# Kernel optimization log

Hardware: AMD Instinct MI355X
Metric: run time of the kernel (lower is better)

The kernel has to match this reference:

```python
import jax, jax.numpy as jnp
import numpy as np

B, S, D, Fd, M, H, L = 4, 1024, 1024, 4096, 512, 16, 2
HD = D // H
EPS = 1e-5


def _ln(x, s, b):
    m = jnp.mean(x, axis=-1, keepdims=True)
    v = jnp.mean((x - m) ** 2, axis=-1, keepdims=True)
    return (x - m) * jax.lax.rsqrt(v + EPS) * s + b


def _mha(x, Wq, bq, Wk, bk, Wv, bv, Wo, bo):
    b_, s_, _ = x.shape
    Q = (x @ Wq + bq).reshape(b_, s_, H, HD)
    K = (x @ Wk + bk).reshape(b_, s_, H, HD)
    V = (x @ Wv + bv).reshape(b_, s_, H, HD)
    scores = jnp.einsum('bihd,bjhd->bhij', Q, K) / np.sqrt(HD).astype(np.float32)
    w = jax.nn.softmax(scores, axis=-1)
    out = jnp.einsum('bhij,bjhd->bihd', w, V).reshape(b_, s_, D)
    return out @ Wo + bo


def setup_inputs() -> dict:
    key = jax.random.key(0)
    ks = iter(jax.random.split(key, 40))
    w = lambda shape: jax.random.normal(next(ks), shape, jnp.float32) * 0.02
    inp = {
        'x': jax.random.normal(next(ks), (B, S, D), jnp.float32),
        # stacked per-global-layer params [L, ...]
        'Wq': w((L, D, D)), 'bq': jnp.zeros((L, D)),
        'Wk': w((L, D, D)), 'bk': jnp.zeros((L, D)),
        'Wv': w((L, D, D)), 'bv': jnp.zeros((L, D)),
        'Wo': w((L, D, D)), 'bo': jnp.zeros((L, D)),
        'W1': w((L, D, Fd)), 'b1': jnp.zeros((L, Fd)),
        'W2': w((L, Fd, D)), 'b2': jnp.zeros((L, D)),
        'n1s': jnp.ones((L, D)), 'n1b': jnp.zeros((L, D)),
        'n2s': jnp.ones((L, D)), 'n2b': jnp.zeros((L, D)),
        # top-level params
        'ln1s': jnp.ones((D,)), 'ln1b': jnp.zeros((D,)),
        'ln2s': jnp.ones((D,)), 'ln2b': jnp.zeros((D,)),
        'ln3s': jnp.ones((D,)), 'ln3b': jnp.zeros((D,)),
        'Wb': w((D, M)), 'bb': jnp.zeros((M,)),      # backbone stand-in
        'Wm': w((M, D)), 'bm': jnp.zeros((D,)),      # self.linear
        'Wf1': w((D, Fd)), 'bf1': jnp.zeros((Fd,)),  # top feed_forward
        'Wf2': w((Fd, D)), 'bf2': jnp.zeros((D,)),
    }
    return inp


def reference(x, Wq, bq, Wk, bk, Wv, bv, Wo, bo, W1, b1, W2, b2,
              n1s, n1b, n2s, n2b, ln1s, ln1b, ln2s, ln2b, ln3s, ln3b,
              Wb, bb, Wm, bm, Wf1, bf1, Wf2, bf2):
    # dropout is identity (eval mode)
    # global branch: stacked EncoderLayers
    g = x
    for i in range(L):
        a = _mha(g, Wq[i], bq[i], Wk[i], bk[i], Wv[i], bv[i], Wo[i], bo[i])
        g = _ln(g + a, n1s[i], n1b[i])
        ff = jax.nn.relu(g @ W1[i] + b1[i]) @ W2[i] + b2[i]
        g = _ln(g + ff, n2s[i], n2b[i])

    def local(frac):
        st = S // frac
        xs = x[:, -st:, :]
        mo = (xs @ Wb + bb) @ Wm + bm
        y = _ln(xs + mo, ln1s, ln1b)
        return jnp.pad(y, ((0, 0), (S - st, 0), (0, 0)))

    output = g + local(2) + local(4)  # S >= 4 branch
    h = _ln(output + x, ln2s, ln2b)
    ff = jax.nn.relu(output @ Wf1 + bf1) @ Wf2 + bf2
    return _ln(h + ff, ln3s, ln3b)
```

## Files before the change

kernel.cpp:

```cpp
#include <hip/hip_runtime.h>
#include <stdint.h>


typedef short   s16x8 __attribute__((ext_vector_type(8)));
typedef float   f32x4 __attribute__((ext_vector_type(4)));
typedef uint16_t u16x8 __attribute__((ext_vector_type(8)));
typedef uint16_t u16x4 __attribute__((ext_vector_type(4)));

__device__ __forceinline__ float bf2f(uint16_t h) {
    union { uint32_t u; float f; } c; c.u = ((uint32_t)h) << 16; return c.f;
}
__device__ __forceinline__ uint16_t f2bf(float f) {
    union { float f; uint32_t u; } c; c.f = f;
    uint32_t u = c.u;
    u += 0x7fffu + ((u >> 16) & 1u);
    return (uint16_t)(u >> 16);
}

__device__ __forceinline__ void g2l16(const uint16_t* g, uint16_t* l) {
    __builtin_amdgcn_global_load_lds(
        (const __attribute__((address_space(1))) void*)g,
        (__attribute__((address_space(3))) void*)l, 16, 0, 0);
}

template<int MODE, int BN, int BK, int DB>
__global__ __launch_bounds__(256) void gemm_bt(
    const uint16_t* __restrict__ A, const uint16_t* __restrict__ Bt,
    const float* __restrict__ bias0, const float* __restrict__ bias1,
    const float* __restrict__ bias2,
    uint16_t* __restrict__ C0, uint16_t* __restrict__ C1,
    uint16_t* __restrict__ C2,
    int M, int N, int K)
{
    constexpr int JN   = BN / 32;
    constexpr int KS   = BK / 32;
    constexpr int CPR  = BK / 8;
    constexpr int LG   = (BK == 32) ? 2 : 3;
    constexpr int RA   = (128 * BK / 8) / 256;
    constexpr int RB   = (BN  * BK / 8) / 256;
    constexpr int NBUF = DB ? 2 : 1;
    constexpr int STG  = NBUF * (128 + BN) * BK;
    constexpr int EPI  = (MODE == 3) ? 0 : 128 * (BN + 8);
    constexpr int SMEM = (STG > EPI) ? STG : EPI;
    __shared__ __align__(16) uint16_t smem[SMEM];
    uint16_t* sAp = smem;
    uint16_t* sBp = smem + NBUF * 128 * BK;

    const int t    = threadIdx.x;
    const int w    = t >> 6;
    const int lane = t & 63;
    const int qd   = lane >> 4;
    const int cc   = lane & 15;

    int bm, bn;
    {
        int gx = gridDim.x, gy = gridDim.y;
        if ((gy & 7) == 0) {
            int id   = blockIdx.y * gx + blockIdx.x;
            int gpg  = gy >> 3;
            int rest = id >> 3;
            bm = (id & 7) * gpg + rest % gpg;
            bn = rest / gpg;
        } else { bm = blockIdx.y; bn = blockIdx.x; }
    }
    const int m0 = bm * 128;
    const int n0 = bn * BN;
    const int wm = (w >> 1) * 64;
    const int wn = (w & 1) * (BN / 2);

    auto key = [](int row) -> int {
        return (BK == 32) ? ((row >> 1) & 3) : (row & 7);
    };

    f32x4 acc[4][JN];
#pragma unroll
    for (int i = 0; i < 4; ++i)
#pragma unroll
        for (int j = 0; j < JN; ++j) acc[i][j] = (f32x4)0.0f;

    int rA[RA], kA[RA];
#pragma unroll
    for (int is = 0; is < RA; ++is) {
        int gc = is * 256 + t;
        int row = gc >> LG, ph = gc & (CPR - 1);
        rA[is] = row;
        kA[is] = (ph ^ key(row)) * 8;
    }
    int rB[RB], kB[RB];
#pragma unroll
    for (int is = 0; is < RB; ++is) {
        int gc = is * 256 + t;
        int row = gc >> LG, ph = gc & (CPR - 1);
        rB[is] = row;
        kB[is] = (ph ^ key(row)) * 8;
    }
    int offA[4][KS], offB[JN][KS];
#pragma unroll
    for (int i = 0; i < 4; ++i) {
        int ml = wm + i * 16 + cc;
#pragma unroll
        for (int ks = 0; ks < KS; ++ks)
            offA[i][ks] = ml * BK + ((ks * 4 + qd) ^ key(ml)) * 8;
    }
#pragma unroll
    for (int j = 0; j < JN; ++j) {
        int nl = wn + j * 16 + cc;
#pragma unroll
        for (int ks = 0; ks < KS; ++ks)
            offB[j][ks] = nl * BK + ((ks * 4 + qd) ^ key(nl)) * 8;
    }

    auto stage = [&](int kt, int buf) {
#pragma unroll
        for (int is = 0; is < RA; ++is)
            g2l16(A + (size_t)(m0 + rA[is]) * K + kt + kA[is],
                  sAp + (size_t)buf * 128 * BK + (size_t)(is * 256 + w * 64) * 8);
#pragma unroll
        for (int is = 0; is < RB; ++is)
            g2l16(Bt + (size_t)(n0 + rB[is]) * K + kt + kB[is],
                  sBp + (size_t)buf * BN * BK + (size_t)(is * 256 + w * 64) * 8);
    };
    auto compute = [&](int buf) {
        const uint16_t* sa = sAp + (size_t)buf * 128 * BK;
        const uint16_t* sb = sBp + (size_t)buf * BN * BK;
#pragma unroll
        for (int ks = 0; ks < KS; ++ks) {
            s16x8 af[4], bv[JN];
#pragma unroll
            for (int i = 0; i < 4; ++i) af[i] = *(const s16x8*)(sa + offA[i][ks]);
#pragma unroll
            for (int j = 0; j < JN; ++j) bv[j] = *(const s16x8*)(sb + offB[j][ks]);
#pragma unroll
            for (int i = 0; i < 4; ++i)
#pragma unroll
                for (int j = 0; j < JN; ++j)
                    acc[i][j] = __builtin_amdgcn_mfma_f32_16x16x32_bf16(
                        af[i], bv[j], acc[i][j], 0, 0, 0);
        }
    };

    if (DB) {
        stage(0, 0);
        __syncthreads();
        int cur = 0;
        for (int kt = 0; kt < K; kt += BK) {
            if (kt + BK < K) stage(kt + BK, cur ^ 1);
            compute(cur);
            __syncthreads();
            cur ^= 1;
        }
    } else {
        for (int kt = 0; kt < K; kt += BK) {
            stage(kt, 0);
            __syncthreads();
            compute(0);
            __syncthreads();
        }
    }

    if (MODE == 3) {
#pragma unroll
        for (int j = 0; j < JN; ++j) {
            int col = n0 + wn + j * 16 + cc;
            int seg = col >> 10;
            const float* bp = (seg == 0) ? bias0 : (seg == 1) ? bias1 : bias2;
            float bb = bp[col & 1023];
#pragma unroll
            for (int i = 0; i < 4; ++i) {
                f32x4 v = acc[i][j];
#pragma unroll
                for (int r = 0; r < 4; ++r) {
                    float val = v[r] + bb;
                    int row = m0 + wm + i * 16 + qd * 4 + r;
                    if (col < 1024) {
                        C0[(size_t)row * 1024 + col] = f2bf(val);
                    } else if (col < 2048) {
                        C1[(size_t)row * 1024 + (col - 1024)] = f2bf(val);
                    } else {
                        int c = col - 2048;
                        int b = row >> 10, s = row & 1023;
                        int hh = c >> 6, d = c & 63;
                        C2[((size_t)(b * 16 + hh) * 64 + d) * 1024 + s] = f2bf(val);
                    }
                }
            }
        }
    } else {
        constexpr int ST = BN + 8;
#pragma unroll
        for (int j = 0; j < JN; ++j) {
            int col = wn + j * 16 + cc;
            float bb = bias0[n0 + col];
#pragma unroll
            for (int i = 0; i < 4; ++i) {
                f32x4 v = acc[i][j];
#pragma unroll
                for (int r = 0; r < 4; ++r) {
                    float val = v[r] + bb;
                    if (MODE == 1) val = fmaxf(val, 0.0f);
                    smem[(wm + i * 16 + qd * 4 + r) * ST + col] = f2bf(val);
                }
            }
        }
        __syncthreads();
        constexpr int NP  = 128 * BN / 2048;
        constexpr int TPR = BN / 8;
#pragma unroll
        for (int p = 0; p < NP; ++p) {
            int row  = p * (256 / TPR) + t / TPR;
            int colc = (t % TPR) * 8;
            u16x8 v = *(const u16x8*)(smem + row * ST + colc);
            *(u16x8*)(C0 + (size_t)(m0 + row) * N + n0 + colc) = v;
        }
    }
}

#define FA_P 76
__global__ __launch_bounds__(256) void flash_attn(
    const uint16_t* __restrict__ Q, const uint16_t* __restrict__ K,
    const uint16_t* __restrict__ Vt, uint16_t* __restrict__ O)
{
    __shared__ __align__(16) uint16_t Qs[64 * FA_P];
    __shared__ __align__(16) uint16_t Ks[64 * FA_P];
    __shared__ __align__(16) uint16_t Vs[64 * FA_P];
    __shared__ __align__(16) uint16_t Ps[64 * FA_P];

    const int t    = threadIdx.x;
    const int w    = t >> 6;
    const int lane = t & 63;
    const int qd   = lane >> 4;
    const int cc   = lane & 15;
    const int id   = blockIdx.x;
    const int xg   = id & 7;
    const int loc  = id >> 3;
    const int bh   = xg * 8 + (loc >> 4);
    const int qblk = loc & 15;
    const int b    = bh >> 4, hh = bh & 15;
    const size_t rowbase = (size_t)b * 1024;

#pragma unroll
    for (int is = 0; is < 2; ++is) {
        int c = is * 256 + t, r = c >> 3, ch = c & 7;
        *(u16x8*)(Qs + r * FA_P + ch * 8) =
            *(const u16x8*)(Q + (rowbase + qblk * 64 + r) * 1024 + hh * 64 + ch * 8);
    }

    f32x4 o[4];
    float lrow[4] = {0.0f, 0.0f, 0.0f, 0.0f};
#pragma unroll
    for (int j = 0; j < 4; ++j) o[j] = (f32x4)0.0f;

    for (int kb = 0; kb < 1024; kb += 64) {
        __syncthreads();
#pragma unroll
        for (int is = 0; is < 2; ++is) {
            int c = is * 256 + t, r = c >> 3, ch = c & 7;
            *(u16x8*)(Ks + r * FA_P + ch * 8) =
                *(const u16x8*)(K + (rowbase + kb + r) * 1024 + hh * 64 + ch * 8);
            *(u16x8*)(Vs + r * FA_P + ch * 8) =
                *(const u16x8*)(Vt + ((size_t)(bh * 64 + r)) * 1024 + kb + ch * 8);
        }
        __syncthreads();

        f32x4 sc[4];
        s16x8 aq0 = *(const s16x8*)(Qs + (w * 16 + cc) * FA_P + qd * 8);
        s16x8 aq1 = *(const s16x8*)(Qs + (w * 16 + cc) * FA_P + 32 + qd * 8);
#pragma unroll
        for (int j = 0; j < 4; ++j) {
            s16x8 b0 = *(const s16x8*)(Ks + (j * 16 + cc) * FA_P + qd * 8);
            s16x8 b1 = *(const s16x8*)(Ks + (j * 16 + cc) * FA_P + 32 + qd * 8);
            sc[j] = __builtin_amdgcn_mfma_f32_16x16x32_bf16(aq0, b0, (f32x4)0.0f, 0, 0, 0);
            sc[j] = __builtin_amdgcn_mfma_f32_16x16x32_bf16(aq1, b1, sc[j], 0, 0, 0);
        }

#pragma unroll
        for (int r = 0; r < 4; ++r) {
            float p0 = __expf(sc[0][r] * 0.125f);
            float p1 = __expf(sc[1][r] * 0.125f);
            float p2 = __expf(sc[2][r] * 0.125f);
            float p3 = __expf(sc[3][r] * 0.125f);
            lrow[r] += (p0 + p1) + (p2 + p3);
            int prow = (w * 16 + qd * 4 + r) * FA_P + cc;
            Ps[prow]      = f2bf(p0);
            Ps[prow + 16] = f2bf(p1);
            Ps[prow + 32] = f2bf(p2);
            Ps[prow + 48] = f2bf(p3);
        }

#pragma unroll
        for (int ks = 0; ks < 2; ++ks) {
            s16x8 ap = *(const s16x8*)(Ps + (w * 16 + cc) * FA_P + ks * 32 + qd * 8);
#pragma unroll
            for (int j = 0; j < 4; ++j) {
                s16x8 bb = *(const s16x8*)(Vs + (j * 16 + cc) * FA_P + ks * 32 + qd * 8);
                o[j] = __builtin_amdgcn_mfma_f32_16x16x32_bf16(ap, bb, o[j], 0, 0, 0);
            }
        }
    }

#pragma unroll
    for (int r = 0; r < 4; ++r) {
        float rs = lrow[r];
        rs += __shfl_xor(rs, 1);
        rs += __shfl_xor(rs, 2);
        rs += __shfl_xor(rs, 4);
        rs += __shfl_xor(rs, 8);
        float inv = 1.0f / rs;
        size_t grow = rowbase + qblk * 64 + w * 16 + qd * 4 + r;
#pragma unroll
        for (int j = 0; j < 4; ++j)
            O[grow * 1024 + hh * 64 + j * 16 + cc] = f2bf(o[j][r] * inv);
    }
}

template<int BT, int F32OUT>
__global__ __launch_bounds__(256) void ln_res(
    const uint16_t* __restrict__ A, const void* __restrict__ Bp,
    const float* __restrict__ S, const float* __restrict__ Bi,
    void* __restrict__ outp)
{
    const int row = blockIdx.x, t = threadIdx.x;
    const int w = t >> 6, lane = t & 63;
    u16x4 a4 = *(const u16x4*)(A + (size_t)row * 1024 + t * 4);
    float bvals[4];
    if (BT == 0) {
        u16x4 b4 = *(const u16x4*)((const uint16_t*)Bp + (size_t)row * 1024 + t * 4);
#pragma unroll
        for (int e = 0; e < 4; ++e) bvals[e] = bf2f(b4[e]);
    } else {
        float4 b4 = *(const float4*)((const float*)Bp + (size_t)row * 1024 + t * 4);
        bvals[0] = b4.x; bvals[1] = b4.y; bvals[2] = b4.z; bvals[3] = b4.w;
    }
    float v[4], sum = 0.0f, sq = 0.0f;
#pragma unroll
    for (int e = 0; e < 4; ++e) {
        v[e] = bf2f(a4[e]) + bvals[e];
        sum += v[e];
        sq  += v[e] * v[e];
    }
#pragma unroll
    for (int d = 1; d < 64; d <<= 1) {
        sum += __shfl_xor(sum, d);
        sq  += __shfl_xor(sq, d);
    }
    __shared__ float rs[4], rq[4];
    if (lane == 0) { rs[w] = sum; rq[w] = sq; }
    __syncthreads();
    sum = rs[0] + rs[1] + rs[2] + rs[3];
    sq  = rq[0] + rq[1] + rq[2] + rq[3];
    float mean = sum * (1.0f / 1024.0f);
    float var  = sq * (1.0f / 1024.0f) - mean * mean;
    float rstd = rsqrtf(var + 1e-5f);
    float4 s4  = *(const float4*)(S + t * 4);
    float4 bi4 = *(const float4*)(Bi + t * 4);
    float r0 = (v[0] - mean) * rstd * s4.x + bi4.x;
    float r1 = (v[1] - mean) * rstd * s4.y + bi4.y;
    float r2 = (v[2] - mean) * rstd * s4.z + bi4.z;
    float r3 = (v[3] - mean) * rstd * s4.w + bi4.w;
    if (F32OUT) {
        *(float4*)((float*)outp + (size_t)row * 1024 + t * 4) =
            make_float4(r0, r1, r2, r3);
    } else {
        u16x4 o4;
        o4[0] = f2bf(r0); o4[1] = f2bf(r1); o4[2] = f2bf(r2); o4[3] = f2bf(r3);
        *(u16x4*)((uint16_t*)outp + (size_t)row * 1024 + t * 4) = o4;
    }
}

__global__ __launch_bounds__(256) void add3(
    const uint16_t* __restrict__ g, const uint16_t* __restrict__ y2,
    const uint16_t* __restrict__ y4, uint16_t* __restrict__ out)
{
    size_t e = ((size_t)blockIdx.x * 256 + threadIdx.x) * 4;
    int row = (int)(e >> 10), col = (int)(e & 1023);
    int b = row >> 10, s = row & 1023;
    u16x4 gv = *(const u16x4*)(g + e);
    float v[4];
#pragma unroll
    for (int k = 0; k < 4; ++k) v[k] = bf2f(gv[k]);
    if (s >= 512) {
        u16x4 a = *(const u16x4*)(y2 + ((size_t)(b * 512 + s - 512)) * 1024 + col);
#pragma unroll
        for (int k = 0; k < 4; ++k) v[k] += bf2f(a[k]);
    }
    if (s >= 768) {
        u16x4 a = *(const u16x4*)(y4 + ((size_t)(b * 256 + s - 768)) * 1024 + col);
#pragma unroll
        for (int k = 0; k < 4; ++k) v[k] += bf2f(a[k]);
    }
    u16x4 o4;
#pragma unroll
    for (int k = 0; k < 4; ++k) o4[k] = f2bf(v[k]);
    *(u16x4*)(out + e) = o4;
}

__global__ __launch_bounds__(256) void copy_rows_f32(
    const float* __restrict__ x, uint16_t* __restrict__ out, int lgst)
{
    size_t e = ((size_t)blockIdx.x * 256 + threadIdx.x) * 4;
    int row = (int)(e >> 10), col = (int)(e & 1023);
    int st = 1 << lgst;
    int b = row >> lgst, s = row & (st - 1);
    float4 a = *(const float4*)(x + ((size_t)(b * 1024 + (1024 - st) + s)) * 1024 + col);
    u16x4 o4;
    o4[0] = f2bf(a.x); o4[1] = f2bf(a.y); o4[2] = f2bf(a.z); o4[3] = f2bf(a.w);
    *(u16x4*)(out + e) = o4;
}

__global__ __launch_bounds__(256) void transpose_k(
    const float* __restrict__ W, uint16_t* __restrict__ Wt, int Kd, int Nd)
{
    __shared__ uint16_t tile[64][68];
    const int t  = threadIdx.x;
    const int n0 = blockIdx.x * 64, k0 = blockIdx.y * 64;
#pragma unroll
    for (int p = 0; p < 4; ++p) {
        int k  = p * 16 + (t >> 4);
        int nn = (t & 15) * 4;
        float4 a = *(const float4*)(W + (size_t)(k0 + k) * Nd + n0 + nn);
        tile[nn + 0][k] = f2bf(a.x);
        tile[nn + 1][k] = f2bf(a.y);
        tile[nn + 2][k] = f2bf(a.z);
        tile[nn + 3][k] = f2bf(a.w);
    }
    __syncthreads();
#pragma unroll
    for (int p = 0; p < 2; ++p) {
        int nn = p * 32 + (t >> 3);
        int kk = (t & 7) * 8;
        u16x8 o = *(const u16x8*)(&tile[nn][kk]);
        *(u16x8*)(Wt + (size_t)(n0 + nn) * Kd + k0 + kk) = o;
    }
}

__global__ __launch_bounds__(256) void cvt(
    const float* __restrict__ src, uint16_t* __restrict__ dst)
{
    size_t i = ((size_t)blockIdx.x * 256 + threadIdx.x) * 8;
    float4 a = *(const float4*)(src + i);
    float4 b = *(const float4*)(src + i + 4);
    u16x8 o;
    o[0] = f2bf(a.x); o[1] = f2bf(a.y); o[2] = f2bf(a.z); o[3] = f2bf(a.w);
    o[4] = f2bf(b.x); o[5] = f2bf(b.y); o[6] = f2bf(b.z); o[7] = f2bf(b.w);
    *(u16x8*)(dst + i) = o;
}

extern "C" void kernel_launch(void* const* d_in, const int* in_sizes, int n_in,
                              void* d_out, int out_size, void* d_ws, size_t ws_size,
                              hipStream_t stream)
{
    const float* x    = (const float*)d_in[0];
    const float* Wq   = (const float*)d_in[1];
    const float* bq   = (const float*)d_in[2];
    const float* Wk   = (const float*)d_in[3];
    const float* bk   = (const float*)d_in[4];
    const float* Wv   = (const float*)d_in[5];
    const float* bv   = (const float*)d_in[6];
    const float* Wo   = (const float*)d_in[7];
    const float* bo   = (const float*)d_in[8];
    const float* W1   = (const float*)d_in[9];
    const float* b1   = (const float*)d_in[10];
    const float* W2   = (const float*)d_in[11];
    const float* b2   = (const float*)d_in[12];
    const float* n1s  = (const float*)d_in[13];
    const float* n1b  = (const float*)d_in[14];
    const float* n2s  = (const float*)d_in[15];
    const float* n2b  = (const float*)d_in[16];
    const float* ln1s = (const float*)d_in[17];
    const float* ln1b = (const float*)d_in[18];
    const float* ln2s = (const float*)d_in[19];
    const float* ln2b = (const float*)d_in[20];
    const float* ln3s = (const float*)d_in[21];
    const float* ln3b = (const float*)d_in[22];
    const float* Wb   = (const float*)d_in[23];
    const float* bb   = (const float*)d_in[24];
    const float* Wm   = (const float*)d_in[25];
    const float* bm   = (const float*)d_in[26];
    const float* Wf1  = (const float*)d_in[27];
    const float* bf1  = (const float*)d_in[28];
    const float* Wf2  = (const float*)d_in[29];
    const float* bf2  = (const float*)d_in[30];

    char* ws = (char*)d_ws;
    const size_t MB = (size_t)1 << 20;
    uint16_t* g    = (uint16_t*)(ws);
    uint16_t* tb   = (uint16_t*)(ws + 8 * MB);
    char*     big  = ws + 16 * MB;
    uint16_t* qb   = (uint16_t*)(big);
    uint16_t* kbuf = (uint16_t*)(big + 8 * MB);
    uint16_t* vtb  = (uint16_t*)(big + 16 * MB);
    uint16_t* ob   = (uint16_t*)(big + 24 * MB);
    uint16_t* ffb  = (uint16_t*)(big);
    uint16_t* xbf  = (uint16_t*)(ws + 48 * MB);
    uint16_t* hb   = (uint16_t*)(ws + 48 * MB);
    uint16_t* wT   = (uint16_t*)(ws + 56 * MB);

    auto T = [&](const float* Wsrc, int Kd, int Nd, uint16_t* dst) {
        transpose_k<<<dim3(Nd / 64, Kd / 64), 256, 0, stream>>>(Wsrc, dst, Kd, Nd);
    };

    cvt<<<2048, 256, 0, stream>>>(x, xbf);

    const uint16_t* gin = xbf;
    for (int i = 0; i < 2; ++i) {
        const size_t wOff = (size_t)i * 1024 * 1024;
        const size_t fOff = (size_t)i * 1024 * 4096;
        T(Wq + wOff, 1024, 1024, wT);
        T(Wk + wOff, 1024, 1024, wT + (size_t)1024 * 1024);
        T(Wv + wOff, 1024, 1024, wT + (size_t)2048 * 1024);
        gemm_bt<3, 128, 32, 1><<<dim3(24, 32), 256, 0, stream>>>(
            gin, wT, bq + i * 1024, bk + i * 1024, bv + i * 1024,
            qb, kbuf, vtb, 4096, 3072, 1024);
        flash_attn<<<1024, 256, 0, stream>>>(qb, kbuf, vtb, ob);
        T(Wo + wOff, 1024, 1024, wT);
        gemm_bt<0, 64, 64, 1><<<dim3(16, 32), 256, 0, stream>>>(
            ob, wT, bo + i * 1024, nullptr, nullptr, tb, nullptr, nullptr,
            4096, 1024, 1024);
        ln_res<0, 0><<<4096, 256, 0, stream>>>(gin, tb, n1s + i * 1024, n1b + i * 1024, g);
        T(W1 + fOff, 1024, 4096, wT);
        gemm_bt<1, 128, 32, 1><<<dim3(32, 32), 256, 0, stream>>>(
            g, wT, b1 + i * 4096, nullptr, nullptr, ffb, nullptr, nullptr,
            4096, 4096, 1024);
        T(W2 + fOff, 4096, 1024, wT);
        gemm_bt<0, 64, 64, 1><<<dim3(16, 32), 256, 0, stream>>>(
            ffb, wT, b2 + i * 1024, nullptr, nullptr, tb, nullptr, nullptr,
            4096, 1024, 4096);
        ln_res<0, 0><<<4096, 256, 0, stream>>>(g, tb, n2s + i * 1024, n2b + i * 1024, g);
        gin = g;
    }

    uint16_t* xsc = (uint16_t*)(big);
    uint16_t* lk  = (uint16_t*)(big + 8 * MB);
    uint16_t* mo  = (uint16_t*)(big + 16 * MB);
    uint16_t* yy  = (uint16_t*)(big + 24 * MB);
    copy_rows_f32<<<2048, 256, 0, stream>>>(x, xsc, 9);
    copy_rows_f32<<<1024, 256, 0, stream>>>(x, xsc + (size_t)2048 * 1024, 8);
    uint16_t* WbT = wT;
    uint16_t* WmT = wT + (size_t)512 * 1024;
    T(Wb, 1024, 512, WbT);
    T(Wm, 512, 1024, WmT);
    gemm_bt<0, 64, 64, 1><<<dim3(8, 24), 256, 0, stream>>>(
        xsc, WbT, bb, nullptr, nullptr, lk, nullptr, nullptr, 3072, 512, 1024);
    gemm_bt<0, 64, 64, 1><<<dim3(16, 24), 256, 0, stream>>>(
        lk, WmT, bm, nullptr, nullptr, mo, nullptr, nullptr, 3072, 1024, 512);
    ln_res<0, 0><<<3072, 256, 0, stream>>>(xsc, mo, ln1s, ln1b, yy);
    uint16_t* y2 = yy;
    uint16_t* y4 = yy + (size_t)2048 * 1024;

    add3<<<4096, 256, 0, stream>>>(g, y2, y4, g);
    ln_res<1, 0><<<4096, 256, 0, stream>>>(g, x, ln2s, ln2b, hb);
    T(Wf1, 1024, 4096, wT);
    gemm_bt<1, 128, 32, 1><<<dim3(32, 32), 256, 0, stream>>>(
        g, wT, bf1, nullptr, nullptr, ffb, nullptr, nullptr, 4096, 4096, 1024);
    T(Wf2, 4096, 1024, wT);
    gemm_bt<0, 64, 64, 1><<<dim3(16, 32), 256, 0, stream>>>(
        ffb, wT, bf2, nullptr, nullptr, tb, nullptr, nullptr, 4096, 1024, 4096);
    ln_res<0, 1><<<4096, 256, 0, stream>>>(hb, tb, ln3s, ln3b, d_out);
}
```

Measured before the change: 802.7 us.

## Add 256x256-tile 512-thread GEMM with 4-stage pipeline for QKV and FFN1

Adds a new GEMM kernel with 256x256 output tiles, 8 waves, a 4-deep global-to-LDS ring buffer with XOR-swizzled layout, staggered A/B staging interleaved with MFMA phases, and an LDS-staged coalesced epilogue. It replaces the 128-wide tile GEMM for the fused QKV projection and the two K=1024 FFN up-projections. The goal is more data reuse per tile and better overlap of loads with MFMA work. The trade-off is fewer workgroups (192/256) on a 256-CU part, which may leave CUs idle, plus heavy register and LDS use.

```diff
diff --git a/kernel.cpp b/kernel.cpp
--- a/kernel.cpp
+++ b/kernel.cpp
@@ -21,6 +21,195 @@
     __builtin_amdgcn_global_load_lds(
         (const __attribute__((address_space(1))) void*)g,
         (__attribute__((address_space(3))) void*)l, 16, 0, 0);
+}
+
+template<int MODE>
+__global__ __launch_bounds__(512, 2) void gemm256(
+    const uint16_t* __restrict__ A, const uint16_t* __restrict__ Bt,
+    const float* __restrict__ bias0, const float* __restrict__ bias1,
+    const float* __restrict__ bias2,
+    uint16_t* __restrict__ C0, uint16_t* __restrict__ C1,
+    uint16_t* __restrict__ C2,
+    int N)
+{
+    __shared__ __align__(16) uint16_t smem[65536];
+    uint16_t* sA = smem;
+    uint16_t* sB = smem + 32768;
+
+    const int tid  = threadIdx.x;
+    const int lane = tid & 63;
+    const int w    = tid >> 6;
+    const int qd   = lane >> 4;
+    const int cc   = lane & 15;
+    const int wmg  = w >> 2;
+    const int wni  = w & 3;
+    const int wn   = wni * 64;
+    const int wb   = tid & ~63;
+
+    const int nwg = gridDim.x;
+    const int cpx = nwg >> 3;
+    const int id  = blockIdx.x;
+    const int wg  = (id & 7) * cpx + (id >> 3);
+    const int bm  = wg & 15;
+    const int bn  = wg >> 4;
+    const int m0  = bm * 256;
+    const int n0  = bn * 256;
+
+    const float* bp = bias0;
+    int n0c = n0;
+    if (MODE == 3) {
+        int seg = n0 >> 10;
+        n0c = n0 & 1023;
+        bp = (seg == 0) ? bias0 : (seg == 1) ? bias1 : bias2;
+    }
+    float bb[4];
+#pragma unroll
+    for (int j = 0; j < 4; ++j) bb[j] = bp[n0c + wn + j * 16 + cc];
+
+    int offA[8], offB[4];
+#pragma unroll
+    for (int i = 0; i < 8; ++i) {
+        int ml = wmg * 128 + i * 16 + cc;
+        offA[i] = ml * 32 + ((qd ^ ((ml >> 1) & 3)) * 8);
+    }
+#pragma unroll
+    for (int j = 0; j < 4; ++j) {
+        int nl = wn + j * 16 + cc;
+        offB[j] = nl * 32 + ((qd ^ ((nl >> 1) & 3)) * 8);
+    }
+
+    int rS[2], kS[2];
+#pragma unroll
+    for (int is = 0; is < 2; ++is) {
+        int gc = is * 512 + tid;
+        int row = gc >> 2, ph = gc & 3;
+        rS[is] = row;
+        kS[is] = (ph ^ ((row >> 1) & 3)) * 8;
+    }
+    auto stA = [&](int tt) {
+        uint16_t* d = sA + (tt & 3) * 8192;
+        int kt = tt * 32;
+#pragma unroll
+        for (int is = 0; is < 2; ++is)
+            g2l16(A + (size_t)(m0 + rS[is]) * 1024 + kt + kS[is],
+                  d + (size_t)(is * 512 + wb) * 8);
+    };
+    auto stB = [&](int tt) {
+        uint16_t* d = sB + (tt & 3) * 8192;
+        int kt = tt * 32;
+#pragma unroll
+        for (int is = 0; is < 2; ++is)
+            g2l16(Bt + (size_t)(n0 + rS[is]) * 1024 + kt + kS[is],
+                  d + (size_t)(is * 512 + wb) * 8);
+    };
+
+    f32x4 acc[8][4];
+#pragma unroll
+    for (int i = 0; i < 8; ++i)
+#pragma unroll
+        for (int j = 0; j < 4; ++j) acc[i][j] = (f32x4)0.0f;
+
+    stA(0); stB(0); stA(1); stB(1); stA(2); stB(2);
+    asm volatile("s_waitcnt vmcnt(8)" ::: "memory");
+    __builtin_amdgcn_s_barrier();
+
+    s16x8 bv[4];
+#pragma unroll 1
+    for (int t = 0; t < 32; ++t) {
+        const uint16_t* sa = sA + (t & 3) * 8192;
+        const uint16_t* sb = sB + (t & 3) * 8192;
+        if (t < 29) stA(t + 3);
+        s16x8 av[4];
+#pragma unroll
+        for (int j = 0; j < 4; ++j) bv[j] = *(const s16x8*)(sb + offB[j]);
+#pragma unroll
+        for (int i = 0; i < 4; ++i) av[i] = *(const s16x8*)(sa + offA[i]);
+        __builtin_amdgcn_s_barrier();
+        asm volatile("s_waitcnt lgkmcnt(0)" ::: "memory");
+        __builtin_amdgcn_sched_barrier(0);
+        __builtin_amdgcn_s_setprio(1);
+#pragma unroll
+        for (int i = 0; i < 4; ++i)
+#pragma unroll
+            for (int j = 0; j < 4; ++j)
+                acc[i][j] = __builtin_amdgcn_mfma_f32_16x16x32_bf16(
+                    av[i], bv[j], acc[i][j], 0, 0, 0);
+        __builtin_amdgcn_s_setprio(0);
+        __builtin_amdgcn_s_barrier();
+        if (t < 29) stB(t + 3);
+#pragma unroll
+        for (int i = 0; i < 4; ++i) av[i] = *(const s16x8*)(sa + offA[4 + i]);
+        __builtin_amdgcn_s_barrier();
+        asm volatile("s_waitcnt lgkmcnt(0)" ::: "memory");
+        __builtin_amdgcn_sched_barrier(0);
+        __builtin_amdgcn_s_setprio(1);
+#pragma unroll
+        for (int i = 0; i < 4; ++i)
+#pragma unroll
+            for (int j = 0; j < 4; ++j)
+                acc[4 + i][j] = __builtin_amdgcn_mfma_f32_16x16x32_bf16(
+                    av[i], bv[j], acc[4 + i][j], 0, 0, 0);
+        __builtin_amdgcn_s_setprio(0);
+        if (t < 29)       { asm volatile("s_waitcnt vmcnt(8)" ::: "memory"); }
+        else if (t == 29) { asm volatile("s_waitcnt vmcnt(4)" ::: "memory"); }
+        else if (t == 30) { asm volatile("s_waitcnt vmcnt(0)" ::: "memory"); }
+        __builtin_amdgcn_s_barrier();
+    }
+
+    if (MODE == 3 && (n0 >> 10) == 2) {
+#pragma unroll
+        for (int j = 0; j < 4; ++j) {
+            int c = n0c + wn + j * 16 + cc;
+            int hh = c >> 6, d = c & 63;
+#pragma unroll
+            for (int i = 0; i < 8; ++i) {
+                int rb = m0 + wmg * 128 + i * 16 + qd * 4;
+                int b = rb >> 10, s = rb & 1023;
+                u16x4 o;
+#pragma unroll
+                for (int r = 0; r < 4; ++r) o[r] = f2bf(acc[i][j][r] + bb[j]);
+                *(u16x4*)(C2 + ((size_t)((b * 16 + hh) * 64 + d)) * 1024 + s) = o;
+            }
+        }
+        return;
+    }
+    {
+        uint16_t* C = C0;
+        int Nc = N;
+        if (MODE == 3) {
+            int seg = n0 >> 10;
+            C = (seg == 0) ? C0 : C1;
+            Nc = 1024;
+        }
+        constexpr int ST = 264;
+#pragma unroll
+        for (int h = 0; h < 2; ++h) {
+            if (wmg == h) {
+#pragma unroll
+                for (int i = 0; i < 8; ++i)
+#pragma unroll
+                    for (int j = 0; j < 4; ++j) {
+                        f32x4 v = acc[i][j];
+#pragma unroll
+                        for (int r = 0; r < 4; ++r) {
+                            float val = v[r] + bb[j];
+                            if (MODE == 1) val = fmaxf(val, 0.0f);
+                            smem[(i * 16 + qd * 4 + r) * ST + wn + j * 16 + cc] =
+                                f2bf(val);
+                        }
+                    }
+            }
+            __syncthreads();
+#pragma unroll
+            for (int p = 0; p < 8; ++p) {
+                int row  = p * 16 + (tid >> 5);
+                int colc = (tid & 31) * 8;
+                u16x8 v = *(const u16x8*)(smem + row * ST + colc);
+                *(u16x8*)(C + (size_t)(m0 + h * 128 + row) * Nc + n0c + colc) = v;
+            }
+            __syncthreads();
+        }
+    }
 }
 
 template<int MODE, int BN, int BK, int DB>
@@ -508,9 +697,9 @@
         T(Wq + wOff, 1024, 1024, wT);
         T(Wk + wOff, 1024, 1024, wT + (size_t)1024 * 1024);
         T(Wv + wOff, 1024, 1024, wT + (size_t)2048 * 1024);
-        gemm_bt<3, 128, 32, 1><<<dim3(24, 32), 256, 0, stream>>>(
+        gemm256<3><<<192, 512, 0, stream>>>(
             gin, wT, bq + i * 1024, bk + i * 1024, bv + i * 1024,
-            qb, kbuf, vtb, 4096, 3072, 1024);
+            qb, kbuf, vtb, 3072);
         flash_attn<<<1024, 256, 0, stream>>>(qb, kbuf, vtb, ob);
         T(Wo + wOff, 1024, 1024, wT);
         gemm_bt<0, 64, 64, 1><<<dim3(16, 32), 256, 0, stream>>>(
@@ -518,9 +707,8 @@
             4096, 1024, 1024);
         ln_res<0, 0><<<4096, 256, 0, stream>>>(gin, tb, n1s + i * 1024, n1b + i * 1024, g);
         T(W1 + fOff, 1024, 4096, wT);
-        gemm_bt<1, 128, 32, 1><<<dim3(32, 32), 256, 0, stream>>>(
-            g, wT, b1 + i * 4096, nullptr, nullptr, ffb, nullptr, nullptr,
-            4096, 4096, 1024);
+        gemm256<1><<<256, 512, 0, stream>>>(
+            g, wT, b1 + i * 4096, nullptr, nullptr, ffb, nullptr, nullptr, 4096);
         T(W2 + fOff, 4096, 1024, wT);
         gemm_bt<0, 64, 64, 1><<<dim3(16, 32), 256, 0, stream>>>(
             ffb, wT, b2 + i * 1024, nullptr, nullptr, tb, nullptr, nullptr,
@@ -550,8 +738,8 @@
     add3<<<4096, 256, 0, stream>>>(g, y2, y4, g);
     ln_res<1, 0><<<4096, 256, 0, stream>>>(g, x, ln2s, ln2b, hb);
     T(Wf1, 1024, 4096, wT);
-    gemm_bt<1, 128, 32, 1><<<dim3(32, 32), 256, 0, stream>>>(
-        g, wT, bf1, nullptr, nullptr, ffb, nullptr, nullptr, 4096, 4096, 1024);
+    gemm256<1><<<256, 512, 0, stream>>>(
+        g, wT, bf1, nullptr, nullptr, ffb, nullptr, nullptr, 4096);
     T(Wf2, 4096, 1024, wT);
     gemm_bt<0, 64, 64, 1><<<dim3(16, 32), 256, 0, stream>>>(
         ffb, wT, bf2, nullptr, nullptr, tb, nullptr, nullptr, 4096, 1024, 4096);
```

Result: no change. 800.4 us (-0.3%).
